# Performance work log

Measured on AMD Instinct MI355X. Metric: run time of the kernel, lower is better.

Reference implementation:

```python
import jax, jax.numpy as jnp
import numpy as np

N = 50000   # nodes
E = 800000  # edges
G = 64      # graphs in batch
D = 128     # joint_embed_dim
H = D // 2  # 64
NEG_SLOPE = 0.2


def _segment_softmax(logits, seg, n):
    m = jax.ops.segment_max(logits, seg, num_segments=n)
    m = jnp.where(jnp.isfinite(m), m, 0.0)
    e = jnp.exp(logits - m[seg])
    s = jax.ops.segment_sum(e, seg, num_segments=n)
    return e / (s[seg] + 1e-16)


def _gat_conv(x, src, dst, W, a_src, a_dst, b, n):
    # PyG GATConv, heads=1, add_self_loops=True
    loops = jnp.arange(n, dtype=src.dtype)
    s = jnp.concatenate([src, loops])
    d = jnp.concatenate([dst, loops])
    h = x @ W                                   # [n, out]
    alpha_s = h @ a_src                         # [n]
    alpha_d = h @ a_dst
    logit = jax.nn.leaky_relu(alpha_s[s] + alpha_d[d], NEG_SLOPE)  # [E+n]
    alpha = _segment_softmax(logit, d, n)
    out = jax.ops.segment_sum(h[s] * alpha[:, None], d, num_segments=n)
    return out + b


def _edge_conv(x, src, dst, We1, be1, We2, be2, n):
    # PyG EdgeConv: max_j nn(cat[x_i, x_j - x_i])
    xi = x[dst]
    xj = x[src]
    feats = jnp.concatenate([xi, xj - xi], axis=1)     # [E, 2*H]
    m = jax.nn.relu(feats @ We1 + be1)
    m = jax.nn.relu(m @ We2 + be2)
    out = jax.ops.segment_max(m, dst, num_segments=n)
    return jnp.where(jnp.isfinite(out), out, 0.0)


def setup_inputs() -> dict:
    key = jax.random.key(0)
    ks = jax.random.split(key, 24)
    x = jax.random.normal(ks[0], (N, 3), dtype=jnp.float32)
    edge_index = jax.random.randint(ks[1], (2, E), 0, N, dtype=jnp.int64)
    batch_ids = jnp.sort(jax.random.randint(ks[2], (N,), 0, G, dtype=jnp.int64))

    def w(k, shape, fan_in):
        return jax.random.normal(k, shape, dtype=jnp.float32) * (1.0 / np.sqrt(fan_in))

    inp = {
        "x": x, "edge_index": edge_index, "batch_ids": batch_ids,
        # GATConv1: 3 -> 64
        "W1": w(ks[3], (3, H), 3), "a1s": w(ks[4], (H,), H), "a1d": w(ks[5], (H,), H), "b1": jnp.zeros((H,), jnp.float32),
        # GATConv2: 64 -> 64
        "W2": w(ks[6], (H, H), H), "a2s": w(ks[7], (H,), H), "a2d": w(ks[8], (H,), H), "b2": jnp.zeros((H,), jnp.float32),
        # GATConv3: 128 -> 128
        "W3": w(ks[9], (D, D), D), "a3s": w(ks[10], (D,), D), "a3d": w(ks[11], (D,), D), "b3": jnp.zeros((D,), jnp.float32),
        # EdgeConv nn: 128 -> 128 -> 128
        "We1": w(ks[12], (D, D), D), "be1": jnp.zeros((D,), jnp.float32),
        "We2": w(ks[13], (D, D), D), "be2": jnp.zeros((D,), jnp.float32),
        # MLP: 256 -> 128 -> 128
        "Wm1": w(ks[14], (2 * D, D), 2 * D), "bm1": jnp.zeros((D,), jnp.float32),
        "Wm2": w(ks[15], (D, D), D), "bm2": jnp.zeros((D,), jnp.float32),
    }
    return inp


def reference(x, edge_index, batch_ids,
              W1, a1s, a1d, b1, W2, a2s, a2d, b2, W3, a3s, a3d, b3,
              We1, be1, We2, be2, Wm1, bm1, Wm2, bm2):
    src, dst = edge_index[0], edge_index[1]
    n = x.shape[0]
    # conv1 + relu (dropout is identity in eval)
    h = jax.nn.relu(_gat_conv(x, src, dst, W1, a1s, a1d, b1, n))
    # conv2 + elu
    h = jax.nn.elu(_gat_conv(h, src, dst, W2, a2s, a2d, b2, n))
    # edge_conv: 64 -> 128
    h = _edge_conv(h, src, dst, We1, be1, We2, be2, n)
    # conv3 + relu
    h = jax.nn.relu(_gat_conv(h, src, dst, W3, a3s, a3d, b3, n))
    # global mean / max pool over graphs
    sums = jax.ops.segment_sum(h, batch_ids, num_segments=G)
    cnts = jax.ops.segment_sum(jnp.ones((n, 1), h.dtype), batch_ids, num_segments=G)
    mean_pool = sums / jnp.maximum(cnts, 1.0)
    max_pool = jax.ops.segment_max(h, batch_ids, num_segments=G)
    max_pool = jnp.where(jnp.isfinite(max_pool), max_pool, 0.0)
    z = jnp.concatenate([mean_pool, max_pool], axis=1)    # [G, 256]
    z = jax.nn.relu(z @ Wm1 + bm1)
    z = jax.nn.relu(z @ Wm2 + bm2)
    norm = jnp.linalg.norm(z, axis=1, keepdims=True)
    return z / jnp.maximum(norm, 1e-12)
```

## Files before the change

kernel.cpp:

```cpp
#include <hip/hip_runtime.h>
#include <hip/hip_bf16.h>
#include <math.h>


typedef __attribute__((ext_vector_type(4))) float f32x4;
typedef __attribute__((ext_vector_type(8))) short bf16x8;
typedef __attribute__((ext_vector_type(8))) ushort u16x8;
typedef short s16x2 __attribute__((ext_vector_type(2)));

__device__ __forceinline__ float wave_sum(float v) {
#pragma unroll
  for (int o = 32; o > 0; o >>= 1) v += __shfl_xor(v, o, 64);
  return v;
}
__device__ __forceinline__ float wave_max(float v) {
#pragma unroll
  for (int o = 32; o > 0; o >>= 1) v = fmaxf(v, __shfl_xor(v, o, 64));
  return v;
}
__device__ __forceinline__ float lrelu(float x) { return x >= 0.f ? x : 0.2f * x; }
__device__ __forceinline__ ushort f2bf(float f) {
  union { float f; unsigned u; } v; v.f = f;
  unsigned r = (v.u + 0x7fff + ((v.u >> 16) & 1)) >> 16;
  return (ushort)r;
}
__device__ __forceinline__ float bf2f(ushort u) {
  union { unsigned u; float f; } v; v.u = ((unsigned)u) << 16;
  return v.f;
}
__device__ __forceinline__ float bflo(unsigned v) { return __uint_as_float(v << 16); }
__device__ __forceinline__ float bfhi(unsigned v) { return __uint_as_float(v & 0xffff0000u); }
__device__ __forceinline__ unsigned pack2bf(float a, float b) {
  __hip_bfloat162 h = __float22bfloat162_rn(make_float2(a, b));
  union { __hip_bfloat162 h; unsigned u; } cv;
  cv.h = h;
  return cv.u;
}
__device__ __forceinline__ unsigned bfadd2_relu(unsigned a, unsigned b) {
  union { unsigned u; __hip_bfloat162 h; s16x2 s; } ua, ub, ur;
  ua.u = a;
  ub.u = b;
  ur.h = __hadd2(ua.h, ub.h);
  s16x2 z = (s16x2)0;
  ur.s = __builtin_elementwise_max(ur.s, z);
  return ur.u;
}


__global__ void count_kernel(const int* __restrict__ ei, int* __restrict__ deg, int E) {
  int e = blockIdx.x * 256 + threadIdx.x;
  if (e < E) atomicAdd(&deg[ei[E + e]], 1);
}

__global__ void scan_local(const int* __restrict__ deg, int* __restrict__ off,
                           int* __restrict__ bsum, int n) {
  __shared__ int buf[256];
  int i = blockIdx.x * 256 + threadIdx.x;
  int v = (i < n) ? deg[i] : 0;
  buf[threadIdx.x] = v;
  __syncthreads();
  int incl = v;
  for (int o = 1; o < 256; o <<= 1) {
    int t = (threadIdx.x >= o) ? buf[threadIdx.x - o] : 0;
    __syncthreads();
    incl += t;
    buf[threadIdx.x] = incl;
    __syncthreads();
  }
  if (i < n) off[i] = incl - v;
  if (threadIdx.x == 255) bsum[blockIdx.x] = incl;
}

__global__ void scan_bsum(int* __restrict__ bsum, int nb) {
  __shared__ int buf[256];
  int v = (threadIdx.x < nb) ? bsum[threadIdx.x] : 0;
  buf[threadIdx.x] = v;
  __syncthreads();
  int incl = v;
  for (int o = 1; o < 256; o <<= 1) {
    int t = (threadIdx.x >= o) ? buf[threadIdx.x - o] : 0;
    __syncthreads();
    incl += t;
    buf[threadIdx.x] = incl;
    __syncthreads();
  }
  if (threadIdx.x < nb) bsum[threadIdx.x] = incl - v;
}

__global__ void scan_add(int* __restrict__ off, const int* __restrict__ bsum, int n, int total) {
  int i = blockIdx.x * 256 + threadIdx.x;
  if (i < n) off[i] += bsum[blockIdx.x];
  if (i == 0) off[n] = total;
}

__global__ void scatter_kernel(const int* __restrict__ ei, const int* __restrict__ off,
                               int* __restrict__ cursor, int* __restrict__ csr_src,
                               int* __restrict__ csr_dst, int E) {
  int e = blockIdx.x * 256 + threadIdx.x;
  if (e < E) {
    int d = ei[E + e];
    int pos = off[d] + atomicAdd(&cursor[d], 1);
    csr_src[pos] = ei[e];
    csr_dst[pos] = d;
  }
}


template <int IN, int OUT>
__global__ __launch_bounds__(256) void node_linear_kernel(
    const float* __restrict__ x, const float* __restrict__ W,
    const float* __restrict__ av_s, const float* __restrict__ av_d,
    ushort* __restrict__ hb, float* __restrict__ as_out, float* __restrict__ ad_out, int n) {
  constexpr int NC = OUT / 64;
  constexpr int NB = 4;
  __shared__ float Wl[IN * OUT];
  if constexpr ((IN * OUT) % 1024 == 0) {
    for (int i = threadIdx.x; i < IN * OUT / 4; i += 256)
      ((float4*)Wl)[i] = ((const float4*)W)[i];
  } else {
    for (int i = threadIdx.x; i < IN * OUT; i += 256) Wl[i] = W[i];
  }
  __syncthreads();
  const int wid = threadIdx.x >> 6, lane = threadIdx.x & 63;
  const int n0 = (blockIdx.x * 4 + wid) * NB;
  if (n0 >= n) return;
  float acc[NB][NC];
#pragma unroll
  for (int j = 0; j < NB; ++j)
#pragma unroll
    for (int c = 0; c < NC; ++c) acc[j][c] = 0.f;
  int nidx[NB];
#pragma unroll
  for (int j = 0; j < NB; ++j) nidx[j] = min(n0 + j, n - 1);

  if constexpr ((IN & 3) == 0) {
#pragma unroll 2
    for (int k = 0; k < IN; k += 4) {
      float4 xv[NB];
#pragma unroll
      for (int j = 0; j < NB; ++j) xv[j] = *(const float4*)&x[nidx[j] * IN + k];
#pragma unroll
      for (int kk = 0; kk < 4; ++kk) {
        float w[NC];
        if constexpr (NC == 2) {
          float2 wv = *(const float2*)&Wl[(k + kk) * OUT + 2 * lane];
          w[0] = wv.x;
          w[1] = wv.y;
        } else {
          w[0] = Wl[(k + kk) * OUT + lane];
        }
#pragma unroll
        for (int j = 0; j < NB; ++j) {
          float xk = (kk == 0) ? xv[j].x : (kk == 1) ? xv[j].y : (kk == 2) ? xv[j].z : xv[j].w;
#pragma unroll
          for (int c = 0; c < NC; ++c) acc[j][c] += xk * w[c];
        }
      }
    }
  } else {
    for (int k = 0; k < IN; ++k) {
      float w[NC];
#pragma unroll
      for (int c = 0; c < NC; ++c) w[c] = (NC == 2) ? Wl[k * OUT + 2 * lane + c] : Wl[k * OUT + lane];
#pragma unroll
      for (int j = 0; j < NB; ++j) {
        float xk = x[nidx[j] * IN + k];
#pragma unroll
        for (int c = 0; c < NC; ++c) acc[j][c] += xk * w[c];
      }
    }
  }

  float a_sv[NC], a_dv[NC];
#pragma unroll
  for (int c = 0; c < NC; ++c) {
    const int col = (NC == 2) ? 2 * lane + c : lane;
    a_sv[c] = av_s[col];
    a_dv[c] = av_d[col];
  }
#pragma unroll
  for (int j = 0; j < NB; ++j) {
    int node = n0 + j;
    if (node >= n) break;
    float ps = 0.f, pd = 0.f;
#pragma unroll
    for (int c = 0; c < NC; ++c) {
      ps += acc[j][c] * a_sv[c];
      pd += acc[j][c] * a_dv[c];
    }
    if constexpr (NC == 2) {
      unsigned pk = pack2bf(acc[j][0], acc[j][1]);
      *(unsigned*)&hb[(size_t)node * OUT + 2 * lane] = pk;
    } else {
      hb[(size_t)node * OUT + lane] = f2bf(acc[j][0]);
    }
    ps = wave_sum(ps);
    pd = wave_sum(pd);
    if (lane == 0) {
      as_out[node] = ps;
      ad_out[node] = pd;
    }
  }
}


template <int K>
__global__ void compute_wa(const float* __restrict__ W, const float* __restrict__ a_s,
                           const float* __restrict__ a_d, float* __restrict__ wa_s,
                           float* __restrict__ wa_d) {
  const int k = threadIdx.x;
  float s = 0.f, d = 0.f;
  for (int j = 0; j < K; ++j) {
    const float w = W[k * K + j];
    s += w * a_s[j];
    d += w * a_d[j];
  }
  wa_s[k] = s;
  wa_d[k] = d;
}


#define NT 64
#define M1S 136
#define M2S 132

__global__ __launch_bounds__(256, 4) void node_mfma_kernel(
    const float* __restrict__ x, const ushort* __restrict__ Wcm,
    const float* __restrict__ wa_s, const float* __restrict__ wa_d,
    ushort* __restrict__ hb, float* __restrict__ as_out, float* __restrict__ ad_out, int n) {
  __shared__ __align__(16) char smem[NT * M2S * 4];
  __shared__ float swa[128], swd[128];
  ushort* m1 = (ushort*)smem;
  float* m2 = (float*)smem;
  const int tid = threadIdx.x;
  const int lane = tid & 63, wid = tid >> 6;
  const int quad = lane >> 4, l16 = lane & 15;
  const int row = tid >> 2, c0 = (tid & 3) * 32;

  bf16x8 bfrag[2][4];
#pragma unroll
  for (int ct = 0; ct < 2; ++ct) {
    const int nn = wid * 32 + ct * 16 + l16;
#pragma unroll
    for (int ks = 0; ks < 4; ++ks)
      bfrag[ct][ks] = *(const bf16x8*)&Wcm[nn * 128 + ks * 32 + quad * 8];
  }
  if (tid < 128) {
    swa[tid] = wa_s[tid];
    swd[tid] = wa_d[tid];
  }
  __syncthreads();

  const int n0 = blockIdx.x * NT;
  const int node = min(n0 + row, n - 1);

  float ps = 0.f, pd = 0.f;
  {
    const float4* xp = (const float4*)&x[(size_t)node * 128 + c0];
#pragma unroll
    for (int i = 0; i < 4; ++i) {
      const float4 a = xp[2 * i], b = xp[2 * i + 1];
      const float4 wa0 = *(const float4*)&swa[c0 + 8 * i];
      const float4 wa1 = *(const float4*)&swa[c0 + 8 * i + 4];
      const float4 wd0 = *(const float4*)&swd[c0 + 8 * i];
      const float4 wd1 = *(const float4*)&swd[c0 + 8 * i + 4];
      ps += a.x * wa0.x + a.y * wa0.y + a.z * wa0.z + a.w * wa0.w
          + b.x * wa1.x + b.y * wa1.y + b.z * wa1.z + b.w * wa1.w;
      pd += a.x * wd0.x + a.y * wd0.y + a.z * wd0.z + a.w * wd0.w
          + b.x * wd1.x + b.y * wd1.y + b.z * wd1.z + b.w * wd1.w;
      uint4 rr;
      rr.x = pack2bf(a.x, a.y);
      rr.y = pack2bf(a.z, a.w);
      rr.z = pack2bf(b.x, b.y);
      rr.w = pack2bf(b.z, b.w);
      *((uint4*)&m1[row * M1S + c0] + i) = rr;
    }
  }
  ps += __shfl_xor(ps, 1, 64);
  ps += __shfl_xor(ps, 2, 64);
  pd += __shfl_xor(pd, 1, 64);
  pd += __shfl_xor(pd, 2, 64);
  if ((tid & 3) == 0 && n0 + row < n) {
    as_out[n0 + row] = ps;
    ad_out[n0 + row] = pd;
  }
  __syncthreads();

  f32x4 acc[4][2];
#pragma unroll
  for (int rt = 0; rt < 4; ++rt)
#pragma unroll
    for (int ct = 0; ct < 2; ++ct) acc[rt][ct] = (f32x4)0.f;
#pragma unroll
  for (int ks = 0; ks < 4; ++ks) {
    bf16x8 afr[4];
#pragma unroll
    for (int rt = 0; rt < 4; ++rt)
      afr[rt] = *(const bf16x8*)&m1[(rt * 16 + l16) * M1S + ks * 32 + quad * 8];
#pragma unroll
    for (int rt = 0; rt < 4; ++rt)
#pragma unroll
      for (int ct = 0; ct < 2; ++ct)
        acc[rt][ct] = __builtin_amdgcn_mfma_f32_16x16x32_bf16(afr[rt], bfrag[ct][ks],
                                                              acc[rt][ct], 0, 0, 0);
  }
  __syncthreads();

#pragma unroll
  for (int ct = 0; ct < 2; ++ct) {
    const int col = wid * 32 + ct * 16 + l16;
#pragma unroll
    for (int rt = 0; rt < 4; ++rt)
#pragma unroll
      for (int r = 0; r < 4; ++r) {
        const int rr2 = rt * 16 + quad * 4 + r;
        m2[rr2 * M2S + col] = acc[rt][ct][r];
      }
  }
  __syncthreads();

  unsigned* hbu = (unsigned*)hb;
#pragma unroll
  for (int i = 0; i < 16; ++i) {
    const int r = wid + 4 * i;
    if (n0 + r < n)
      hbu[(size_t)(n0 + r) * 64 + lane] =
          pack2bf(m2[r * M2S + 2 * lane], m2[r * M2S + 2 * lane + 1]);
  }
}


#define M1S64 72
#define M2S64 68

__global__ __launch_bounds__(256, 4) void node_mfma64_kernel(
    const float* __restrict__ x, const ushort* __restrict__ Wcm,
    const float* __restrict__ wa_s, const float* __restrict__ wa_d,
    ushort* __restrict__ hb, float* __restrict__ as_out, float* __restrict__ ad_out, int n) {
  __shared__ __align__(16) char smem[NT * M2S64 * 4];
  __shared__ float swa[64], swd[64];
  ushort* m1 = (ushort*)smem;
  float* m2 = (float*)smem;
  const int tid = threadIdx.x;
  const int lane = tid & 63, wid = tid >> 6;
  const int quad = lane >> 4, l16 = lane & 15;
  const int row = tid >> 2, c0 = (tid & 3) * 16;

  bf16x8 bfrag[2];
#pragma unroll
  for (int ks = 0; ks < 2; ++ks)
    bfrag[ks] = *(const bf16x8*)&Wcm[(wid * 16 + l16) * 64 + ks * 32 + quad * 8];
  if (tid < 64) {
    swa[tid] = wa_s[tid];
    swd[tid] = wa_d[tid];
  }
  __syncthreads();

  const int n0 = blockIdx.x * NT;
  const int node = min(n0 + row, n - 1);

  float ps = 0.f, pd = 0.f;
  {
    const float4* xp = (const float4*)&x[(size_t)node * 64 + c0];
#pragma unroll
    for (int i = 0; i < 2; ++i) {
      const float4 a = xp[2 * i], b = xp[2 * i + 1];
      const float4 wa0 = *(const float4*)&swa[c0 + 8 * i];
      const float4 wa1 = *(const float4*)&swa[c0 + 8 * i + 4];
      const float4 wd0 = *(const float4*)&swd[c0 + 8 * i];
      const float4 wd1 = *(const float4*)&swd[c0 + 8 * i + 4];
      ps += a.x * wa0.x + a.y * wa0.y + a.z * wa0.z + a.w * wa0.w
          + b.x * wa1.x + b.y * wa1.y + b.z * wa1.z + b.w * wa1.w;
      pd += a.x * wd0.x + a.y * wd0.y + a.z * wd0.z + a.w * wd0.w
          + b.x * wd1.x + b.y * wd1.y + b.z * wd1.z + b.w * wd1.w;
      uint4 rr;
      rr.x = pack2bf(a.x, a.y);
      rr.y = pack2bf(a.z, a.w);
      rr.z = pack2bf(b.x, b.y);
      rr.w = pack2bf(b.z, b.w);
      *((uint4*)&m1[row * M1S64 + c0] + i) = rr;
    }
  }
  ps += __shfl_xor(ps, 1, 64);
  ps += __shfl_xor(ps, 2, 64);
  pd += __shfl_xor(pd, 1, 64);
  pd += __shfl_xor(pd, 2, 64);
  if ((tid & 3) == 0 && n0 + row < n) {
    as_out[n0 + row] = ps;
    ad_out[n0 + row] = pd;
  }
  __syncthreads();

  f32x4 acc[4];
#pragma unroll
  for (int rt = 0; rt < 4; ++rt) acc[rt] = (f32x4)0.f;
#pragma unroll
  for (int ks = 0; ks < 2; ++ks) {
    bf16x8 afr[4];
#pragma unroll
    for (int rt = 0; rt < 4; ++rt)
      afr[rt] = *(const bf16x8*)&m1[(rt * 16 + l16) * M1S64 + ks * 32 + quad * 8];
#pragma unroll
    for (int rt = 0; rt < 4; ++rt)
      acc[rt] = __builtin_amdgcn_mfma_f32_16x16x32_bf16(afr[rt], bfrag[ks], acc[rt], 0, 0, 0);
  }
  __syncthreads();

  {
    const int col = wid * 16 + l16;
#pragma unroll
    for (int rt = 0; rt < 4; ++rt)
#pragma unroll
      for (int r = 0; r < 4; ++r) {
        const int rr2 = rt * 16 + quad * 4 + r;
        m2[rr2 * M2S64 + col] = acc[rt][r];
      }
  }
  __syncthreads();

  unsigned* hbu = (unsigned*)hb;
#pragma unroll
  for (int i = 0; i < 8; ++i) {
    const int r = wid * 2 + (lane >> 5) + 8 * i;
    const int j = lane & 31;
    if (n0 + r < n)
      hbu[(size_t)(n0 + r) * 32 + j] =
          pack2bf(m2[r * M2S64 + 2 * j], m2[r * M2S64 + 2 * j + 1]);
  }
}


template <int OUT, int ACT>
__global__ __launch_bounds__(256) void gat_agg_kernel(
    const ushort* __restrict__ h, const float* __restrict__ as_, const float* __restrict__ ad_,
    const float* __restrict__ bias, const int* __restrict__ off, const int* __restrict__ csr_src,
    float* __restrict__ out, int n) {
  constexpr int NC = OUT / 64;
  __shared__ float wbuf[4][64];
  __shared__ int sbuf[4][64];
  const int wid = threadIdx.x >> 6, lane = threadIdx.x & 63;
  const int d = blockIdx.x * 4 + wid;
  if (d >= n) return;
  const int s0 = off[d], s1 = off[d + 1];
  const float ad = ad_[d];
  const float l_self = lrelu(as_[d] + ad);
  unsigned selfv = 0;
  ushort selfu = 0;
  if constexpr (NC == 2)
    selfv = *(const unsigned*)&h[(size_t)d * OUT + 2 * lane];
  else
    selfu = h[(size_t)d * OUT + lane];

  float m = l_self;
  float esum_l = 0.f;
  float acc[NC];
#pragma unroll
  for (int c = 0; c < NC; ++c) acc[c] = 0.f;

  for (int base = s0; base < s1; base += 64) {
    const int cnt = min(64, s1 - base);
    const int idx = base + lane;
    float l = -3.0e38f;
    int s_l = 0;
    if (idx < s1) {
      s_l = csr_src[idx];
      l = lrelu(as_[s_l] + ad);
    }
    const float cm = wave_max(l);
    if (cm > m) {
      const float alpha = __expf(m - cm);
      esum_l *= alpha;
#pragma unroll
      for (int c = 0; c < NC; ++c) acc[c] *= alpha;
      m = cm;
    }
    const float w_l = (idx < s1) ? __expf(l - m) : 0.f;
    sbuf[wid][lane] = s_l;
    wbuf[wid][lane] = w_l;
    esum_l += w_l;
    __threadfence_block();
    int j = 0;
    for (; j + 8 <= cnt; j += 8) {
      float w[8];
      int a[8];
#pragma unroll
      for (int t = 0; t < 8; ++t) {
        w[t] = wbuf[wid][j + t];
        a[t] = sbuf[wid][j + t];
      }
      if constexpr (NC == 2) {
        unsigned v[8];
#pragma unroll
        for (int t = 0; t < 8; ++t) v[t] = *(const unsigned*)&h[(size_t)a[t] * OUT + 2 * lane];
#pragma unroll
        for (int t = 0; t < 8; ++t) {
          acc[0] += w[t] * bflo(v[t]);
          acc[1] += w[t] * bfhi(v[t]);
        }
      } else {
        ushort v[8];
#pragma unroll
        for (int t = 0; t < 8; ++t) v[t] = h[(size_t)a[t] * OUT + lane];
#pragma unroll
        for (int t = 0; t < 8; ++t) acc[0] += w[t] * bf2f(v[t]);
      }
    }
    for (; j < cnt; ++j) {
      const float wj = wbuf[wid][j];
      const int aj = sbuf[wid][j];
      if constexpr (NC == 2) {
        const unsigned v = *(const unsigned*)&h[(size_t)aj * OUT + 2 * lane];
        acc[0] += wj * bflo(v);
        acc[1] += wj * bfhi(v);
      } else {
        acc[0] += wj * bf2f(h[(size_t)aj * OUT + lane]);
      }
    }
    __threadfence_block();
  }
  const float self_w = __expf(l_self - m);
  const float esum = wave_sum(esum_l) + self_w;
  if constexpr (NC == 2) {
    acc[0] += self_w * bflo(selfv);
    acc[1] += self_w * bfhi(selfv);
  } else {
    acc[0] += self_w * bf2f(selfu);
  }
  const float inv = 1.f / (esum + 1e-16f);
  if constexpr (NC == 2) {
    float2 o2;
    float v0 = acc[0] * inv + bias[2 * lane];
    float v1 = acc[1] * inv + bias[2 * lane + 1];
    if (ACT == 0) {
      v0 = fmaxf(v0, 0.f);
      v1 = fmaxf(v1, 0.f);
    } else {
      v0 = v0 > 0.f ? v0 : expm1f(v0);
      v1 = v1 > 0.f ? v1 : expm1f(v1);
    }
    o2.x = v0;
    o2.y = v1;
    *(float2*)&out[(size_t)d * OUT + 2 * lane] = o2;
  } else {
    float v = acc[0] * inv + bias[lane];
    if (ACT == 0)
      v = fmaxf(v, 0.f);
    else
      v = v > 0.f ? v : expm1f(v);
    out[(size_t)d * OUT + lane] = v;
  }
}


__global__ __launch_bounds__(256) void pq_kernel(
    const float* __restrict__ x, const float* __restrict__ We1, const float* __restrict__ be1,
    ushort* __restrict__ P, ushort* __restrict__ Q, int n) {
  __shared__ float AmB[64 * 128];
  __shared__ float Bm[64 * 128];
  for (int i = threadIdx.x; i < 64 * 128; i += 256) {
    float b = We1[64 * 128 + i];
    AmB[i] = We1[i] - b;
    Bm[i] = b;
  }
  __syncthreads();
  const int wid = threadIdx.x >> 6, lane = threadIdx.x & 63;
  const int n0 = (blockIdx.x * 4 + wid) * 4;
  if (n0 >= n) return;
  int nidx[4];
#pragma unroll
  for (int j = 0; j < 4; ++j) nidx[j] = min(n0 + j, n - 1);
  float ap[4][2], aq[4][2];
#pragma unroll
  for (int j = 0; j < 4; ++j) { ap[j][0] = ap[j][1] = aq[j][0] = aq[j][1] = 0.f; }
#pragma unroll 2
  for (int k = 0; k < 64; k += 4) {
    float4 xv[4];
#pragma unroll
    for (int j = 0; j < 4; ++j) xv[j] = *(const float4*)&x[nidx[j] * 64 + k];
#pragma unroll
    for (int kk = 0; kk < 4; ++kk) {
      const float wa0 = AmB[(k + kk) * 128 + lane], wa1 = AmB[(k + kk) * 128 + 64 + lane];
      const float wb0 = Bm[(k + kk) * 128 + lane], wb1 = Bm[(k + kk) * 128 + 64 + lane];
#pragma unroll
      for (int j = 0; j < 4; ++j) {
        const float xk = (kk == 0) ? xv[j].x : (kk == 1) ? xv[j].y : (kk == 2) ? xv[j].z : xv[j].w;
        ap[j][0] += xk * wa0;
        ap[j][1] += xk * wa1;
        aq[j][0] += xk * wb0;
        aq[j][1] += xk * wb1;
      }
    }
  }
  const float b0 = be1[lane], b1v = be1[64 + lane];
#pragma unroll
  for (int j = 0; j < 4; ++j) {
    const int node = n0 + j;
    if (node >= n) break;
    P[(size_t)node * 128 + lane] = f2bf(ap[j][0] + b0);
    P[(size_t)node * 128 + 64 + lane] = f2bf(ap[j][1] + b1v);
    Q[(size_t)node * 128 + lane] = f2bf(aq[j][0]);
    Q[(size_t)node * 128 + 64 + lane] = f2bf(aq[j][1]);
  }
}


template <int K>
__global__ void convert_wcm(const float* __restrict__ W, ushort* __restrict__ Wcm) {
  int i = blockIdx.x * 256 + threadIdx.x;
  if (i >= K * K) return;
  int k = i / K, nn = i % K;
  Wcm[nn * K + k] = f2bf(W[k * K + nn]);
}


#define TE 64

__global__ __launch_bounds__(256, 4) void edgeconv_mfma_kernel(
    const int* __restrict__ csr_src, const int* __restrict__ csr_dst,
    const ushort* __restrict__ P, const ushort* __restrict__ Q,
    const ushort* __restrict__ We2cm, const float* __restrict__ be2,
    float* __restrict__ out, int E, int ntiles) {
  __shared__ __align__(16) char smem[TE * M2S * 4];
  __shared__ int didx2[2][TE];
  ushort* m1 = (ushort*)smem;
  float* m2 = (float*)smem;
  const int tid = threadIdx.x;
  const int lane = tid & 63, wid = tid >> 6;
  const int quad = lane >> 4, l16 = lane & 15;
  const int row = tid >> 2;
  const int c0 = (tid & 3) * 32;

  bf16x8 bfrag[2][4];
#pragma unroll
  for (int ct = 0; ct < 2; ++ct) {
    const int nn = wid * 32 + ct * 16 + l16;
#pragma unroll
    for (int ks = 0; ks < 4; ++ks)
      bfrag[ct][ks] = *(const bf16x8*)&We2cm[nn * 128 + ks * 32 + quad * 8];
  }
  const float b0v = be2[wid * 32 + l16];
  const float b1v = be2[wid * 32 + 16 + l16];

  int t = blockIdx.x;
  if (t >= ntiles) return;

  uint4 pv[4], qv[4];
  {
    const int p = t * TE + row;
    int dd = 0, ss = 0;
    if (p < E) { dd = csr_dst[p]; ss = csr_src[p]; }
    const uint4* Pp = (const uint4*)&P[(size_t)dd * 128 + c0];
    const uint4* Qp = (const uint4*)&Q[(size_t)ss * 128 + c0];
#pragma unroll
    for (int i = 0; i < 4; ++i) { pv[i] = Pp[i]; qv[i] = Qp[i]; }
  }
  if (tid < TE) {
    const int p = t * TE + tid;
    didx2[0][tid] = (p < E) ? csr_dst[p] : -1;
  }

  int buf = 0;
  for (; t < ntiles; t += gridDim.x, buf ^= 1) {
    __syncthreads();

#pragma unroll
    for (int i = 0; i < 4; ++i) {
      uint4 rr;
      rr.x = bfadd2_relu(pv[i].x, qv[i].x);
      rr.y = bfadd2_relu(pv[i].y, qv[i].y);
      rr.z = bfadd2_relu(pv[i].z, qv[i].z);
      rr.w = bfadd2_relu(pv[i].w, qv[i].w);
      *((uint4*)&m1[row * M1S + c0] + i) = rr;
    }

    const int tn = t + gridDim.x;
    const bool hasNext = (tn < ntiles);
    int ddn = 0, ssn = 0;
    if (hasNext) {
      const int p = tn * TE + row;
      if (p < E) { ddn = csr_dst[p]; ssn = csr_src[p]; }
      if (tid < TE) {
        const int p2 = tn * TE + tid;
        didx2[buf ^ 1][tid] = (p2 < E) ? csr_dst[p2] : -1;
      }
    }
    __syncthreads();

    f32x4 acc[4][2];
#pragma unroll
    for (int rt = 0; rt < 4; ++rt)
#pragma unroll
      for (int ct = 0; ct < 2; ++ct) acc[rt][ct] = (f32x4)0.f;
#pragma unroll
    for (int ks = 0; ks < 4; ++ks) {
      bf16x8 afr[4];
#pragma unroll
      for (int rt = 0; rt < 4; ++rt)
        afr[rt] = *(const bf16x8*)&m1[(rt * 16 + l16) * M1S + ks * 32 + quad * 8];
#pragma unroll
      for (int rt = 0; rt < 4; ++rt)
#pragma unroll
        for (int ct = 0; ct < 2; ++ct)
          acc[rt][ct] = __builtin_amdgcn_mfma_f32_16x16x32_bf16(afr[rt], bfrag[ct][ks],
                                                                acc[rt][ct], 0, 0, 0);
    }

    if (hasNext) {
      const uint4* Pp = (const uint4*)&P[(size_t)ddn * 128 + c0];
      const uint4* Qp = (const uint4*)&Q[(size_t)ssn * 128 + c0];
#pragma unroll
      for (int i = 0; i < 4; ++i) { pv[i] = Pp[i]; qv[i] = Qp[i]; }
    }
    __syncthreads();

#pragma unroll
    for (int ct = 0; ct < 2; ++ct) {
      const int col = wid * 32 + ct * 16 + l16;
      const float b = ct == 0 ? b0v : b1v;
#pragma unroll
      for (int rt = 0; rt < 4; ++rt)
#pragma unroll
        for (int r = 0; r < 4; ++r) {
          const int rr2 = rt * 16 + quad * 4 + r;
          m2[rr2 * M2S + col] = fmaxf(acc[rt][ct][r] + b, 0.f);
        }
    }
    __syncthreads();

    const int col = tid & 127;
    const int r0 = (tid >> 7) * 32, r1 = r0 + 32;
    float runmax = 0.f;
    int cur = didx2[buf][r0];
    for (int r = r0; r < r1; ++r) {
      const int dd = didx2[buf][r];
      if (dd != cur) {
        if (cur >= 0) atomicMax((int*)&out[(size_t)cur * 128 + col], __float_as_int(runmax));
        cur = dd;
        runmax = 0.f;
      }
      runmax = fmaxf(runmax, m2[r * M2S + col]);
    }
    if (cur >= 0) atomicMax((int*)&out[(size_t)cur * 128 + col], __float_as_int(runmax));
  }
}


__global__ __launch_bounds__(256) void pool_part_kernel(
    const float* __restrict__ h, const int* __restrict__ bid,
    float* __restrict__ psum, float* __restrict__ pmax, int n) {
  const int chunk = (n + gridDim.x - 1) / gridDim.x;
  const int start = blockIdx.x * chunk;
  const int end = min(start + chunk, n);
  if (start >= end) return;
  const int c = threadIdx.x & 127, half = threadIdx.x >> 7;
  float sum = 0.f, mx = 0.f;
  int cur = -1;
  for (int i = start + half; i < end; i += 2) {
    const int g = bid[i];
    if (g != cur) {
      if (cur >= 0) {
        atomicAdd(&psum[cur * 128 + c], sum);
        atomicMax((int*)&pmax[cur * 128 + c], __float_as_int(mx));
      }
      cur = g;
      sum = 0.f;
      mx = 0.f;
    }
    const float v = h[(size_t)i * 128 + c];
    sum += v;
    mx = fmaxf(mx, v);
  }
  if (cur >= 0) {
    atomicAdd(&psum[cur * 128 + c], sum);
    atomicMax((int*)&pmax[cur * 128 + c], __float_as_int(mx));
  }
}


__global__ __launch_bounds__(128) void mlp_kernel(
    const float* __restrict__ psum, const float* __restrict__ pmax,
    const int* __restrict__ bid, int n,
    const float* __restrict__ Wm1, const float* __restrict__ bm1,
    const float* __restrict__ Wm2, const float* __restrict__ bm2,
    float* __restrict__ outp) {
  const int g = blockIdx.x;
  const int c = threadIdx.x;
  __shared__ float zin[256], z1[128];
  __shared__ int scnt;
  if (c == 0) {
    int lo = 0, hi = n;
    while (lo < hi) { int mid = (lo + hi) >> 1; if (bid[mid] < g) lo = mid + 1; else hi = mid; }
    const int start = lo;
    lo = start; hi = n;
    while (lo < hi) { int mid = (lo + hi) >> 1; if (bid[mid] < g + 1) lo = mid + 1; else hi = mid; }
    scnt = lo - start;
  }
  __syncthreads();
  const float invc = 1.f / fmaxf((float)scnt, 1.f);
  zin[c] = psum[g * 128 + c] * invc;
  zin[c + 128] = pmax[g * 128 + c];
  __syncthreads();
  float a = bm1[c];
  for (int k = 0; k < 256; ++k) a += zin[k] * Wm1[k * 128 + c];
  a = fmaxf(a, 0.f);
  z1[c] = a;
  __syncthreads();
  float b = bm2[c];
  for (int k = 0; k < 128; ++k) b += z1[k] * Wm2[k * 128 + c];
  b = fmaxf(b, 0.f);
  float ss = wave_sum(b * b);
  __shared__ float sred[2];
  if ((threadIdx.x & 63) == 0) sred[threadIdx.x >> 6] = ss;
  __syncthreads();
  const float nrm = sqrtf(sred[0] + sred[1]);
  outp[g * 128 + c] = b / fmaxf(nrm, 1e-12f);
}


extern "C" void kernel_launch(void* const* d_in, const int* in_sizes, int n_in, void* d_out,
                              int out_size, void* d_ws, size_t ws_size, hipStream_t stream) {
  const float* x = (const float*)d_in[0];
  const int* ei = (const int*)d_in[1];
  const int* bid = (const int*)d_in[2];
  const float* W1 = (const float*)d_in[3];
  const float* a1s = (const float*)d_in[4];
  const float* a1d = (const float*)d_in[5];
  const float* b1 = (const float*)d_in[6];
  const float* W2 = (const float*)d_in[7];
  const float* a2s = (const float*)d_in[8];
  const float* a2d = (const float*)d_in[9];
  const float* b2 = (const float*)d_in[10];
  const float* W3 = (const float*)d_in[11];
  const float* a3s = (const float*)d_in[12];
  const float* a3d = (const float*)d_in[13];
  const float* b3 = (const float*)d_in[14];
  const float* We1 = (const float*)d_in[15];
  const float* be1 = (const float*)d_in[16];
  const float* We2 = (const float*)d_in[17];
  const float* be2 = (const float*)d_in[18];
  const float* Wm1 = (const float*)d_in[19];
  const float* bm1 = (const float*)d_in[20];
  const float* Wm2 = (const float*)d_in[21];
  const float* bm2v = (const float*)d_in[22];

  const int n = in_sizes[0] / 3;
  const int E = in_sizes[1] / 2;
  const int G = out_size / 128;

  char* w = (char*)d_ws;
  size_t o = 0;
  auto alloc = [&](size_t bytes) {
    void* p = w + o;
    o = (o + bytes + 255) & ~(size_t)255;
    return p;
  };
  int* deg = (int*)alloc((size_t)n * 4);
  int* off = (int*)alloc((size_t)(n + 1) * 4);
  int* bsum = (int*)alloc(1024 * 4);
  int* csr_src = (int*)alloc((size_t)E * 4);
  int* csr_dst = (int*)alloc((size_t)E * 4);
  ushort* We2cm = (ushort*)alloc(128 * 128 * 2);
  ushort* W3cm = (ushort*)alloc(128 * 128 * 2);
  ushort* W2cm = (ushort*)alloc(64 * 64 * 2);
  float* was = (float*)alloc(128 * 4);
  float* wad = (float*)alloc(128 * 4);
  float* wa2s = (float*)alloc(64 * 4);
  float* wa2d = (float*)alloc(64 * 4);
  float* as_ = (float*)alloc((size_t)n * 4);
  float* ad_ = (float*)alloc((size_t)n * 4);
  ushort* T64 = (ushort*)alloc((size_t)n * 64 * 2);
  float* X64 = (float*)alloc((size_t)n * 64 * 4);
  ushort* Pbf = (ushort*)alloc((size_t)n * 128 * 2);
  ushort* Qbf = (ushort*)alloc((size_t)n * 128 * 2);
  float* H3 = (float*)alloc((size_t)n * 128 * 4);
  float* psum = (float*)alloc((size_t)G * 128 * 4);
  float* pmax = (float*)alloc((size_t)G * 128 * 4);
  (void)ws_size;

  ushort* Hbf = Pbf;
  float* C3out = H3;

  const int nb256 = (n + 255) / 256;
  const int ebl = (E + 255) / 256;
  const int nlb = (n + 15) / 16;
  const int agb = (n + 3) / 4;
  const int ecb = (E + TE - 1) / TE;
  const int nmb = (n + NT - 1) / NT;

  hipMemsetAsync(deg, 0, (size_t)n * 4, stream);
  count_kernel<<<ebl, 256, 0, stream>>>(ei, deg, E);
  scan_local<<<nb256, 256, 0, stream>>>(deg, off, bsum, n);
  scan_bsum<<<1, 256, 0, stream>>>(bsum, nb256);
  scan_add<<<nb256, 256, 0, stream>>>(off, bsum, n, E);
  hipMemsetAsync(deg, 0, (size_t)n * 4, stream);
  scatter_kernel<<<ebl, 256, 0, stream>>>(ei, off, deg, csr_src, csr_dst, E);
  convert_wcm<128><<<64, 256, 0, stream>>>(We2, We2cm);
  convert_wcm<128><<<64, 256, 0, stream>>>(W3, W3cm);
  convert_wcm<64><<<16, 256, 0, stream>>>(W2, W2cm);
  compute_wa<128><<<1, 128, 0, stream>>>(W3, a3s, a3d, was, wad);
  compute_wa<64><<<1, 64, 0, stream>>>(W2, a2s, a2d, wa2s, wa2d);

  node_linear_kernel<3, 64><<<nlb, 256, 0, stream>>>(x, W1, a1s, a1d, T64, as_, ad_, n);
  gat_agg_kernel<64, 0><<<agb, 256, 0, stream>>>(T64, as_, ad_, b1, off, csr_src, X64, n);
  node_mfma64_kernel<<<nmb, 256, 0, stream>>>(X64, W2cm, wa2s, wa2d, T64, as_, ad_, n);
  gat_agg_kernel<64, 1><<<agb, 256, 0, stream>>>(T64, as_, ad_, b2, off, csr_src, X64, n);
  pq_kernel<<<nlb, 256, 0, stream>>>(X64, We1, be1, Pbf, Qbf, n);
  hipMemsetAsync(H3, 0, (size_t)n * 128 * 4, stream);
  edgeconv_mfma_kernel<<<1024, 256, 0, stream>>>(csr_src, csr_dst, Pbf, Qbf, We2cm, be2, H3,
                                                 E, ecb);
  node_mfma_kernel<<<nmb, 256, 0, stream>>>(H3, W3cm, was, wad, Hbf, as_, ad_, n);
  gat_agg_kernel<128, 0><<<agb, 256, 0, stream>>>(Hbf, as_, ad_, b3, off, csr_src, C3out, n);
  hipMemsetAsync(psum, 0, (size_t)G * 128 * 4 * 2, stream);
  pool_part_kernel<<<512, 256, 0, stream>>>(C3out, bid, psum, pmax, n);
  mlp_kernel<<<G, 128, 0, stream>>>(psum, pmax, bid, n, Wm1, bm1, Wm2, bm2v, (float*)d_out);
}
```

Before: 512.0 us.

## Use half-wave per node in 64-dim GAT aggregation and transpose edgeconv max staging

Adds a gat_agg64 kernel that packs two destination nodes per wavefront, with each 32-lane half handling one node using an online softmax and bf16 pair loads. This halves the number of idle lanes for the 64-wide layers. The edgeconv epilogue now stores MFMA results transposed in shared memory with float4 writes, and the segmented max reads destination indices and values as vectors. The goal is to cut LDS instruction count and bank conflicts, at the cost of a larger shared buffer and different unroll behaviour.

```diff
diff --git a/kernel.cpp b/kernel.cpp
--- a/kernel.cpp
+++ b/kernel.cpp
@@ -16,6 +16,16 @@
 __device__ __forceinline__ float wave_max(float v) {
 #pragma unroll
   for (int o = 32; o > 0; o >>= 1) v = fmaxf(v, __shfl_xor(v, o, 64));
+  return v;
+}
+__device__ __forceinline__ float half_sum(float v) {
+#pragma unroll
+  for (int o = 16; o > 0; o >>= 1) v += __shfl_xor(v, o, 64);
+  return v;
+}
+__device__ __forceinline__ float half_max(float v) {
+#pragma unroll
+  for (int o = 16; o > 0; o >>= 1) v = fmaxf(v, __shfl_xor(v, o, 64));
   return v;
 }
 __device__ __forceinline__ float lrelu(float x) { return x >= 0.f ? x : 0.2f * x; }
@@ -552,6 +562,91 @@
 }
 
 
+template <int ACT>
+__global__ __launch_bounds__(256) void gat_agg64_kernel(
+    const ushort* __restrict__ h, const float* __restrict__ as_, const float* __restrict__ ad_,
+    const float* __restrict__ bias, const int* __restrict__ off, const int* __restrict__ csr_src,
+    float* __restrict__ out, int n) {
+  __shared__ float wbuf[4][64];
+  __shared__ int sbuf[4][64];
+  const int wid = threadIdx.x >> 6, lane = threadIdx.x & 63;
+  const int half = lane >> 5, sl = lane & 31;
+  const int d0 = blockIdx.x * 8 + wid * 2 + half;
+  const bool wr = d0 < n;
+  const int d = wr ? d0 : (n - 1);
+  const int s0 = off[d], s1 = off[d + 1];
+  const float ad = ad_[d];
+  const float l_self = lrelu(as_[d] + ad);
+  const unsigned selfv = *(const unsigned*)&h[(size_t)d * 64 + 2 * sl];
+
+  float m = l_self;
+  float esum_l = 0.f, acc0 = 0.f, acc1 = 0.f;
+
+  for (int base = s0; base < s1; base += 32) {
+    const int cnt = min(32, s1 - base);
+    const int idx = base + sl;
+    float l = -3.0e38f;
+    int s_l = 0;
+    if (idx < s1) {
+      s_l = csr_src[idx];
+      l = lrelu(as_[s_l] + ad);
+    }
+    const float cm = half_max(l);
+    const float alpha = (cm > m) ? __expf(m - cm) : 1.f;
+    esum_l *= alpha;
+    acc0 *= alpha;
+    acc1 *= alpha;
+    m = fmaxf(m, cm);
+    const float w_l = (idx < s1) ? __expf(l - m) : 0.f;
+    sbuf[wid][half * 32 + sl] = s_l;
+    wbuf[wid][half * 32 + sl] = w_l;
+    esum_l += w_l;
+    __threadfence_block();
+    int j = 0;
+    for (; j + 8 <= cnt; j += 8) {
+      float w[8];
+      int a[8];
+#pragma unroll
+      for (int t = 0; t < 8; ++t) {
+        w[t] = wbuf[wid][half * 32 + j + t];
+        a[t] = sbuf[wid][half * 32 + j + t];
+      }
+      unsigned v[8];
+#pragma unroll
+      for (int t = 0; t < 8; ++t) v[t] = *(const unsigned*)&h[(size_t)a[t] * 64 + 2 * sl];
+#pragma unroll
+      for (int t = 0; t < 8; ++t) {
+        acc0 += w[t] * bflo(v[t]);
+        acc1 += w[t] * bfhi(v[t]);
+      }
+    }
+    for (; j < cnt; ++j) {
+      const float wj = wbuf[wid][half * 32 + j];
+      const int aj = sbuf[wid][half * 32 + j];
+      const unsigned v = *(const unsigned*)&h[(size_t)aj * 64 + 2 * sl];
+      acc0 += wj * bflo(v);
+      acc1 += wj * bfhi(v);
+    }
+    __threadfence_block();
+  }
+  const float self_w = __expf(l_self - m);
+  const float esum = half_sum(esum_l) + self_w;
+  acc0 += self_w * bflo(selfv);
+  acc1 += self_w * bfhi(selfv);
+  const float inv = 1.f / (esum + 1e-16f);
+  float v0 = acc0 * inv + bias[2 * sl];
+  float v1 = acc1 * inv + bias[2 * sl + 1];
+  if (ACT == 0) {
+    v0 = fmaxf(v0, 0.f);
+    v1 = fmaxf(v1, 0.f);
+  } else {
+    v0 = v0 > 0.f ? v0 : expm1f(v0);
+    v1 = v1 > 0.f ? v1 : expm1f(v1);
+  }
+  if (wr) *(float2*)&out[(size_t)d * 64 + 2 * sl] = make_float2(v0, v1);
+}
+
+
 __global__ __launch_bounds__(256) void pq_kernel(
     const float* __restrict__ x, const float* __restrict__ We1, const float* __restrict__ be1,
     ushort* __restrict__ P, ushort* __restrict__ Q, int n) {
@@ -614,16 +709,17 @@
 
 
 #define TE 64
+#define M2T 68
 
 __global__ __launch_bounds__(256, 4) void edgeconv_mfma_kernel(
     const int* __restrict__ csr_src, const int* __restrict__ csr_dst,
     const ushort* __restrict__ P, const ushort* __restrict__ Q,
     const ushort* __restrict__ We2cm, const float* __restrict__ be2,
     float* __restrict__ out, int E, int ntiles) {
-  __shared__ __align__(16) char smem[TE * M2S * 4];
-  __shared__ int didx2[2][TE];
+  __shared__ __align__(16) char smem[128 * M2T * 4];
+  __shared__ __align__(16) int didx2[2][TE];
   ushort* m1 = (ushort*)smem;
-  float* m2 = (float*)smem;
+  float* m2t = (float*)smem;
   const int tid = threadIdx.x;
   const int lane = tid & 63, wid = tid >> 6;
   const int quad = lane >> 4, l16 = lane & 15;
@@ -718,27 +814,37 @@
       const int col = wid * 32 + ct * 16 + l16;
       const float b = ct == 0 ? b0v : b1v;
 #pragma unroll
-      for (int rt = 0; rt < 4; ++rt)
-#pragma unroll
-        for (int r = 0; r < 4; ++r) {
-          const int rr2 = rt * 16 + quad * 4 + r;
-          m2[rr2 * M2S + col] = fmaxf(acc[rt][ct][r] + b, 0.f);
+      for (int rt = 0; rt < 4; ++rt) {
+        float4 mv;
+        mv.x = fmaxf(acc[rt][ct][0] + b, 0.f);
+        mv.y = fmaxf(acc[rt][ct][1] + b, 0.f);
+        mv.z = fmaxf(acc[rt][ct][2] + b, 0.f);
+        mv.w = fmaxf(acc[rt][ct][3] + b, 0.f);
+        *(float4*)&m2t[col * M2T + rt * 16 + quad * 4] = mv;
+      }
+    }
+    __syncthreads();
+
+    const int col = tid & 127;
+    const int r0 = (tid >> 7) * 32;
+    float runmax = 0.f;
+    int cur = -2;
+#pragma unroll
+    for (int i = 0; i < 8; ++i) {
+      const int4 dv = *(const int4*)&didx2[buf][r0 + 4 * i];
+      const float4 mv = *(const float4*)&m2t[col * M2T + r0 + 4 * i];
+      const int da[4] = {dv.x, dv.y, dv.z, dv.w};
+      const float ma[4] = {mv.x, mv.y, mv.z, mv.w};
+#pragma unroll
+      for (int r = 0; r < 4; ++r) {
+        const int dd = da[r];
+        if (dd != cur) {
+          if (cur >= 0) atomicMax((int*)&out[(size_t)cur * 128 + col], __float_as_int(runmax));
+          cur = dd;
+          runmax = 0.f;
         }
-    }
-    __syncthreads();
-
-    const int col = tid & 127;
-    const int r0 = (tid >> 7) * 32, r1 = r0 + 32;
-    float runmax = 0.f;
-    int cur = didx2[buf][r0];
-    for (int r = r0; r < r1; ++r) {
-      const int dd = didx2[buf][r];
-      if (dd != cur) {
-        if (cur >= 0) atomicMax((int*)&out[(size_t)cur * 128 + col], __float_as_int(runmax));
-        cur = dd;
-        runmax = 0.f;
-      }
-      runmax = fmaxf(runmax, m2[r * M2S + col]);
+        runmax = fmaxf(runmax, ma[r]);
+      }
     }
     if (cur >= 0) atomicMax((int*)&out[(size_t)cur * 128 + col], __float_as_int(runmax));
   }
@@ -884,6 +990,7 @@
   const int ebl = (E + 255) / 256;
   const int nlb = (n + 15) / 16;
   const int agb = (n + 3) / 4;
+  const int agb8 = (n + 7) / 8;
   const int ecb = (E + TE - 1) / TE;
   const int nmb = (n + NT - 1) / NT;
 
@@ -901,9 +1008,9 @@
   compute_wa<64><<<1, 64, 0, stream>>>(W2, a2s, a2d, wa2s, wa2d);
 
   node_linear_kernel<3, 64><<<nlb, 256, 0, stream>>>(x, W1, a1s, a1d, T64, as_, ad_, n);
-  gat_agg_kernel<64, 0><<<agb, 256, 0, stream>>>(T64, as_, ad_, b1, off, csr_src, X64, n);
+  gat_agg64_kernel<0><<<agb8, 256, 0, stream>>>(T64, as_, ad_, b1, off, csr_src, X64, n);
   node_mfma64_kernel<<<nmb, 256, 0, stream>>>(X64, W2cm, wa2s, wa2d, T64, as_, ad_, n);
-  gat_agg_kernel<64, 1><<<agb, 256, 0, stream>>>(T64, as_, ad_, b2, off, csr_src, X64, n);
+  gat_agg64_kernel<1><<<agb8, 256, 0, stream>>>(T64, as_, ad_, b2, off, csr_src, X64, n);
   pq_kernel<<<nlb, 256, 0, stream>>>(X64, We1, be1, Pbf, Qbf, n);
   hipMemsetAsync(H3, 0, (size_t)n * 128 * 4, stream);
   edgeconv_mfma_kernel<<<1024, 256, 0, stream>>>(csr_src, csr_dst, Pbf, Qbf, We2cm, be2, H3,
```

Result: faster. 494.1 us (-3.5%).
